# Kernel optimization log

Hardware: AMD Instinct MI355X
Metric: run time of the kernel (lower is better)

## Reference

```python
import jax, jax.numpy as jnp
import numpy as np

V, N, C, H, W = 4, 65536, 128, 512, 512
M_POOL, K, DH = 1024, 5, 128


def setup_inputs() -> dict:
    key = jax.random.key(0)
    ks = jax.random.split(key, 6)
    points = jax.random.normal(ks[0], (N, 3), dtype=jnp.float32) * 0.3  # human-scale pcd near origin
    zbuffer = 2.0 + jax.random.uniform(ks[1], (V, 1, H, W), dtype=jnp.float32)  # depth ~ camera distance
    feat_map = jax.random.normal(ks[2], (V, C, H, W), dtype=jnp.float32) * 0.1
    image = jax.random.uniform(ks[3], (V, 3, H, W), dtype=jnp.float32)
    # cameras: identity rotation, small x-baseline, looking at origin from z=2.5
    R = jnp.tile(jnp.eye(3, dtype=jnp.float32)[None], (V, 1, 1))
    t = jnp.stack([jnp.array([0.1 * v - 0.15, 0.0, 2.5], dtype=jnp.float32) for v in range(V)])
    extr = jnp.concatenate([R, t[:, :, None]], axis=-1)  # [V,3,4]
    intr = jnp.tile(jnp.array([[700.0, 0.0, W / 2], [0.0, 700.0, H / 2], [0.0, 0.0, 1.0]], dtype=jnp.float32)[None], (V, 1, 1))
    W1 = jax.random.normal(ks[4], (C + 1, DH), dtype=jnp.float32) * 0.05
    b1 = jnp.zeros((DH,), dtype=jnp.float32)
    w2 = jax.random.normal(ks[5], (DH, 1), dtype=jnp.float32) * 0.05
    return dict(points=points, extr=extr, intr=intr, zbuffer=zbuffer,
                feat_map=feat_map, image=image, W1=W1, b1=b1, w2=w2)


def _bilinear(img, u, v):
    """Zero-padded bilinear sample. img [C,H,W]; u,v [N] pixel coords -> [N,C]."""
    Cc, Hh, Ww = img.shape
    u0f = jnp.floor(u); v0f = jnp.floor(v)
    du = u - u0f; dv = v - v0f
    u0 = u0f.astype(jnp.int32); v0 = v0f.astype(jnp.int32)
    out = jnp.zeros((Cc, u.shape[0]), dtype=img.dtype)
    for vi, ui, w in ((v0, u0, (1 - du) * (1 - dv)), (v0, u0 + 1, du * (1 - dv)),
                      (v0 + 1, u0, (1 - du) * dv), (v0 + 1, u0 + 1, du * dv)):
        valid = ((vi >= 0) & (vi < Hh) & (ui >= 0) & (ui < Ww)).astype(img.dtype)
        vals = img[:, jnp.clip(vi, 0, Hh - 1), jnp.clip(ui, 0, Ww - 1)]  # [C,N]
        out = out + vals * (w * valid)[None]
    return out.T  # [N,C]


def _project(points, extr, intr):
    cam = jnp.einsum('vij,nj->vni', extr[:, :, :3], points) + extr[:, None, :, 3]  # [V,N,3]
    depth = cam[..., 2]  # [V,N]
    pix = jnp.einsum('vij,vnj->vni', intr, cam)
    u = pix[..., 0] / (pix[..., 2] + 1e-9)
    v = pix[..., 1] / (pix[..., 2] + 1e-9)
    return u, v, depth


def reference(points, extr, intr, zbuffer, feat_map, image, W1, b1, w2):
    u, v, depth = _project(points, extr, intr)
    sample = jax.vmap(_bilinear)  # over V views
    zbuf = sample(zbuffer, u, v)[..., 0]  # [V,N] sampled z-buffer (0 outside frame)
    out_mask = jnp.any(zbuf == 0.0, axis=0)  # [N] point missing in some view
    # --- KNN inverse-distance zbuf replacement (torch.no_grad block) ---
    pts_sg = jax.lax.stop_gradient(points)
    zbuf_sg = jax.lax.stop_gradient(zbuf)
    cand = pts_sg[:M_POOL]                       # candidate in-point pool
    cand_bad = out_mask[:M_POOL]
    d2 = jnp.sum((pts_sg[:, None, :] - cand[None, :, :]) ** 2, axis=-1)  # [N,M]
    d2 = jnp.where(cand_bad[None, :], jnp.inf, d2)
    negd, idx = jax.lax.top_k(-d2, K)            # K nearest candidates
    dists = jnp.sqrt(jnp.maximum(-negd, 0.0))
    disp = 1.0 / (dists + 1e-8)
    wknn = disp / (jnp.sum(disp, -1, keepdims=True) + 1e-12)  # [N,K]
    replace = jnp.sum(zbuf_sg[:, idx] * wknn[None], -1)       # [V,N]
    zbuf = jnp.where(out_mask[None], replace, zbuf)
    # --- visibility ---
    vis = 1.0 - jnp.abs(zbuf - depth) / (zbuf + 1e-9)  # [V,N]
    # --- multi-view projector sampling + attention fusion (MVF) ---
    feat_s = sample(feat_map, u, v)  # [V,N,C]
    rgb_s = sample(image, u, v)      # [V,N,3]
    x = jnp.concatenate([feat_s, vis[..., None]], -1)          # [V,N,C+1]
    h = jax.nn.relu(jnp.einsum('vnc,cd->vnd', x, W1) + b1)     # [V,N,DH]
    attn = jax.nn.softmax(jnp.einsum('vnd,do->vno', h, w2), axis=0)  # softmax over views
    feat = jnp.sum(attn * feat_s, axis=0)  # [N,C]
    rgb = jnp.sum(attn * rgb_s, axis=0)    # [N,3]
    return jnp.concatenate([feat, rgb], axis=-1)  # [N,C+3]
```

## Files before the change

### kernel.cpp

```cpp
#include <hip/hip_runtime.h>
#include <math.h>

#define NV 4
#define NPT 65536
#define NC 128
#define IMH 512
#define IMW 512
#define MPOOL 1024
#define NDH 128
#define KNN 5
#define NB 8
#define OUTC 131
#define NFLAGS (4 * 512 * 4)

typedef unsigned int uint32;
typedef unsigned short ushort16;
typedef __attribute__((ext_vector_type(8))) short short8v;
typedef __attribute__((ext_vector_type(4))) float float4v;

__device__ inline ushort16 f2bf(float f) {
    uint32 u = __float_as_uint(f);
    u += 0x7fffu + ((u >> 16) & 1u);
    return (ushort16)(u >> 16);
}
__device__ inline float bflo(uint32 a) { return __uint_as_float(a << 16); }
__device__ inline float bfhi(uint32 a) { return __uint_as_float(a & 0xffff0000u); }
__device__ inline float bf1(ushort16 a) { return __uint_as_float(((uint32)a) << 16); }

__global__ void k_wprep(const float* __restrict__ W1, uint4* __restrict__ Bf,
                        int* __restrict__ counter, int* __restrict__ flags) {
    int idx = blockIdx.x * blockDim.x + threadIdx.x;
    if (idx == 0) *counter = 0;
    if (idx < NFLAGS) flags[idx] = 0;
    if (idx >= 5 * 8 * 64) return;
    int l = idx & 63, t = (idx >> 6) & 7, kb = idx >> 9;
    int d = t * 16 + (l & 15);
    uint32 w[4];
#pragma unroll
    for (int p = 0; p < 4; ++p) {
        uint32 lohi = 0;
#pragma unroll
        for (int h = 0; h < 2; ++h) {
            int j = p * 2 + h;
            int k = kb * 32 + (l >> 4) * 8 + j;
            float wv = (k < NC + 1) ? W1[k * NDH + d] : 0.f;
            lohi |= ((uint32)f2bf(wv)) << (16 * h);
        }
        w[p] = lohi;
    }
    Bf[idx] = make_uint4(w[0], w[1], w[2], w[3]);
}

__global__ __launch_bounds__(256)
void k_prep(const float* __restrict__ pts, const float* __restrict__ extr,
            const float* __restrict__ intr, const float* __restrict__ zbuffer,
            float* __restrict__ uarr, float* __restrict__ varr,
            float* __restrict__ darr, float* __restrict__ zarr,
            int* __restrict__ mask, int* __restrict__ list,
            int* __restrict__ counter, int* __restrict__ flags) {
    int n = blockIdx.x * blockDim.x + threadIdx.x;
    if (n >= NPT) return;
    float p0 = pts[3 * n], p1 = pts[3 * n + 1], p2 = pts[3 * n + 2];
    int msk = 0;
#pragma unroll
    for (int v = 0; v < NV; ++v) {
        const float* e = extr + v * 12;
        float c0 = e[0] * p0 + e[1] * p1 + e[2] * p2 + e[3];
        float c1 = e[4] * p0 + e[5] * p1 + e[6] * p2 + e[7];
        float c2 = e[8] * p0 + e[9] * p1 + e[10] * p2 + e[11];
        const float* kk = intr + v * 9;
        float x0 = kk[0] * c0 + kk[1] * c1 + kk[2] * c2;
        float x1 = kk[3] * c0 + kk[4] * c1 + kk[5] * c2;
        float x2 = kk[6] * c0 + kk[7] * c1 + kk[8] * c2;
        float uu = x0 / (x2 + 1e-9f);
        float vv = x1 / (x2 + 1e-9f);
        int vn = v * NPT + n;
        uarr[vn] = uu; varr[vn] = vv; darr[vn] = c2;

        const float* img = zbuffer + (size_t)v * IMH * IMW;
        float u0f = floorf(uu), v0f = floorf(vv);
        float du = uu - u0f, dv = vv - v0f;
        int iu0 = (int)u0f, iv0 = (int)v0f;
        float w00 = (1.f - du) * (1.f - dv);
        float w01 = du * (1.f - dv);
        float w10 = (1.f - du) * dv;
        float w11 = du * dv;
        int iu0c = min(max(iu0, 0), IMW - 1), iu1c = min(max(iu0 + 1, 0), IMW - 1);
        int iv0c = min(max(iv0, 0), IMH - 1), iv1c = min(max(iv0 + 1, 0), IMH - 1);
        float m00 = (iu0 >= 0 && iu0 < IMW && iv0 >= 0 && iv0 < IMH) ? w00 : 0.f;
        float m01 = (iu0 + 1 >= 0 && iu0 + 1 < IMW && iv0 >= 0 && iv0 < IMH) ? w01 : 0.f;
        float m10 = (iu0 >= 0 && iu0 < IMW && iv0 + 1 >= 0 && iv0 + 1 < IMH) ? w10 : 0.f;
        float m11 = (iu0 + 1 >= 0 && iu0 + 1 < IMW && iv0 + 1 >= 0 && iv0 + 1 < IMH) ? w11 : 0.f;
        float z = img[iv0c * IMW + iu0c] * m00 + img[iv0c * IMW + iu1c] * m01 +
                  img[iv1c * IMW + iu0c] * m10 + img[iv1c * IMW + iu1c] * m11;
        zarr[vn] = z;
        msk |= (z == 0.f);

        int base = v * 2048;
        int xt0 = iu0c >> 7, xt1 = iu1c >> 7;
        flags[base + iv0c * 4 + xt0] = 1;
        flags[base + iv0c * 4 + xt1] = 1;
        flags[base + iv1c * 4 + xt0] = 1;
        flags[base + iv1c * 4 + xt1] = 1;
    }
    mask[n] = msk;
    if (msk) {
        int pos = atomicAdd(counter, 1);
        list[pos] = n;
    }
}

__global__ __launch_bounds__(256)
void k_knn_c(const float* __restrict__ pts, const int* __restrict__ mask,
             const int* __restrict__ list, const int* __restrict__ counter,
             float* __restrict__ zarr) {
    __shared__ float cx[MPOOL], cy[MPOOL], cz[MPOOL];
    int count = *counter;
    if ((int)blockIdx.x * 256 >= count) return;
    for (int m = threadIdx.x; m < MPOOL; m += 256) {
        int bad = mask[m];
        cx[m] = bad ? INFINITY : pts[3 * m];
        cy[m] = pts[3 * m + 1];
        cz[m] = pts[3 * m + 2];
    }
    __syncthreads();
    int i = blockIdx.x * 256 + threadIdx.x;
    if (i >= count) return;
    int n = list[i];
    float px = pts[3 * n], py = pts[3 * n + 1], pz = pts[3 * n + 2];
    float bd[KNN];
    int bi[KNN];
#pragma unroll
    for (int k = 0; k < KNN; ++k) { bd[k] = INFINITY; bi[k] = 0; }
    for (int m = 0; m < MPOOL; ++m) {
        float dx = px - cx[m];
        float dy = py - cy[m];
        float dz = pz - cz[m];
        float d = dx * dx + dy * dy + dz * dz;
        int id = m;
#pragma unroll
        for (int k = 0; k < KNN; ++k) {
            if (d < bd[k]) {
                float td = bd[k]; int ti = bi[k];
                bd[k] = d; bi[k] = id;
                d = td; id = ti;
            }
        }
    }
    float disp[KNN];
    float s = 0.f;
#pragma unroll
    for (int k = 0; k < KNN; ++k) {
        float dist = sqrtf(fmaxf(bd[k], 0.f));
        disp[k] = 1.f / (dist + 1e-8f);
        s += disp[k];
    }
    float inv = 1.f / (s + 1e-12f);
#pragma unroll
    for (int v = 0; v < NV; ++v) {
        float r = 0.f;
#pragma unroll
        for (int k = 0; k < KNN; ++k) r += zarr[v * NPT + bi[k]] * (disp[k] * inv);
        zarr[v * NPT + n] = r;
    }
}

__global__ __launch_bounds__(256)
void k_tfeat(const float* __restrict__ feat, ushort16* __restrict__ tfeat,
             const int* __restrict__ flags) {
    __shared__ ushort16 tile[128][130];
    int bid = blockIdx.x;
    int xt = bid & 3;
    int y = (bid >> 2) & 511;
    int v = bid >> 11;
    if (!flags[v * 2048 + y * 4 + xt]) return;
    int x0 = xt * 128;
    int lane = threadIdx.x & 63, wave = threadIdx.x >> 6;
    const size_t HW = (size_t)IMH * IMW;
    const float* src = feat + (size_t)v * NC * HW + (size_t)y * IMW + x0;
#pragma unroll
    for (int i = 0; i < 32; ++i) {
        int c = i * 4 + wave;
        float2 val = *(const float2*)(src + (size_t)c * HW + lane * 2);
        tile[lane * 2][c] = f2bf(val.x);
        tile[lane * 2 + 1][c] = f2bf(val.y);
    }
    __syncthreads();
    uint32* dst = (uint32*)tfeat + ((size_t)v * HW + (size_t)y * IMW + x0) * 64;
#pragma unroll
    for (int i = 0; i < 32; ++i) {
        int pix = i * 4 + wave;
        uint32 val = *(const uint32*)&tile[pix][2 * lane];
        dst[(size_t)pix * 64 + lane] = val;
    }
}

__global__ __launch_bounds__(256)
void k_trgb(const float* __restrict__ image, ushort16* __restrict__ trgb) {
    int bid = blockIdx.x;
    int xt = bid & 1, y = (bid >> 1) & 511, v = bid >> 10;
    int x = xt * 256 + threadIdx.x;
    const size_t HW = (size_t)IMH * IMW;
    size_t p = (size_t)y * IMW + x;
    const float* src = image + (size_t)v * 3 * HW;
    ushort4 o;
    o.x = f2bf(src[p]);
    o.y = f2bf(src[HW + p]);
    o.z = f2bf(src[2 * HW + p]);
    o.w = 0;
    *(ushort4*)(trgb + ((size_t)v * HW + p) * 4) = o;
}

__global__ __launch_bounds__(128)
void k_fused_m(const float* __restrict__ uarr, const float* __restrict__ varr,
               const float* __restrict__ darr, const float* __restrict__ zarr,
               const ushort16* __restrict__ tfeat, const ushort16* __restrict__ trgb,
               const uint4* __restrict__ Bf, const float* __restrict__ b1,
               const float* __restrict__ w2, float* __restrict__ out) {
    const int tid = threadIdx.x;
    const int n0 = blockIdx.x * NB;
    const size_t HW = (size_t)IMH * IMW;
    __shared__ ushort16 fs[32][168];
    __shared__ float rgbs[32][3];
    __shared__ int po[32][4];
    __shared__ float pm[32][4];
    __shared__ float sc[32];
    __shared__ float red[32][2];

    {
        int q = tid >> 2, corner = tid & 3;
        int nb = q >> 2, v = q & 3;
        int vn = v * NPT + n0 + nb;
        float uu = uarr[vn], vv = varr[vn];
        float u0f = floorf(uu), v0f = floorf(vv);
        float du = uu - u0f, dv = vv - v0f;
        int iu0 = (int)u0f, iv0 = (int)v0f;
        float w00 = (1.f - du) * (1.f - dv);
        float w01 = du * (1.f - dv);
        float w10 = (1.f - du) * dv;
        float w11 = du * dv;
        int iu0c = min(max(iu0, 0), IMW - 1), iu1c = min(max(iu0 + 1, 0), IMW - 1);
        int iv0c = min(max(iv0, 0), IMH - 1), iv1c = min(max(iv0 + 1, 0), IMH - 1);
        float m00 = (iu0 >= 0 && iu0 < IMW && iv0 >= 0 && iv0 < IMH) ? w00 : 0.f;
        float m01 = (iu0 + 1 < IMW && iu0 + 1 >= 0 && iv0 >= 0 && iv0 < IMH) ? w01 : 0.f;
        float m10 = (iu0 >= 0 && iu0 < IMW && iv0 + 1 < IMH && iv0 + 1 >= 0) ? w10 : 0.f;
        float m11 = (iu0 + 1 < IMW && iu0 + 1 >= 0 && iv0 + 1 < IMH && iv0 + 1 >= 0) ? w11 : 0.f;
        int oo, iuc, ivc;
        float mm;
        if (corner == 0)      { ivc = iv0c; iuc = iu0c; mm = m00; }
        else if (corner == 1) { ivc = iv0c; iuc = iu1c; mm = m01; }
        else if (corner == 2) { ivc = iv1c; iuc = iu0c; mm = m10; }
        else                  { ivc = iv1c; iuc = iu1c; mm = m11; }
        oo = ivc * IMW + iuc;
        po[q][corner] = oo;
        pm[q][corner] = mm;
        const ushort16* c = trgb + ((size_t)v * HW + oo) * 4;
        float cr = bf1(c[0]) * mm, cg = bf1(c[1]) * mm, cb = bf1(c[2]) * mm;
        cr += __shfl_xor(cr, 1); cr += __shfl_xor(cr, 2);
        cg += __shfl_xor(cg, 1); cg += __shfl_xor(cg, 2);
        cb += __shfl_xor(cb, 1); cb += __shfl_xor(cb, 2);
        if (corner == 0) {
            rgbs[q][0] = cr; rgbs[q][1] = cg; rgbs[q][2] = cb;
            float z = zarr[vn], dd = darr[vn];
            float vis = 1.f - fabsf(z - dd) / (z + 1e-9f);
            fs[q][128] = f2bf(vis);
        }
        for (int k = 129 + corner; k < 168; k += 4) fs[q][k] = 0;
    }
    __syncthreads();

    const uint32* T = (const uint32*)tfeat;
    int sub = tid >> 6, c2 = tid & 63;
#pragma unroll
    for (int i = 0; i < 16; ++i) {
        int q = i * 2 + sub;
        int v = q & 3;
        const uint32* Bv = T + (size_t)v * HW * 64;
        int o0 = po[q][0], o1 = po[q][1], o2 = po[q][2], o3 = po[q][3];
        float m0 = pm[q][0], m1 = pm[q][1], m2 = pm[q][2], m3 = pm[q][3];
        uint32 a0 = Bv[(size_t)o0 * 64 + c2];
        uint32 a1 = Bv[(size_t)o1 * 64 + c2];
        uint32 a2 = Bv[(size_t)o2 * 64 + c2];
        uint32 a3 = Bv[(size_t)o3 * 64 + c2];
        float lo = bflo(a0) * m0 + bflo(a1) * m1 + bflo(a2) * m2 + bflo(a3) * m3;
        float hi = bfhi(a0) * m0 + bfhi(a1) * m1 + bfhi(a2) * m2 + bfhi(a3) * m3;
        uint32 packed = (uint32)f2bf(lo) | ((uint32)f2bf(hi) << 16);
        *(uint32*)&fs[q][2 * c2] = packed;
    }
    __syncthreads();

    const int l = tid & 63, w = tid >> 6;
    const int col = l & 15, kg = l >> 4;
    float4v acc[2][4];
#pragma unroll
    for (int g = 0; g < 2; ++g)
#pragma unroll
        for (int t = 0; t < 4; ++t) acc[g][t] = (float4v){0.f, 0.f, 0.f, 0.f};
#pragma unroll
    for (int kb = 0; kb < 5; ++kb) {
        short8v a0 = *(const short8v*)&fs[col][kb * 32 + kg * 8];
        short8v a1 = *(const short8v*)&fs[16 + col][kb * 32 + kg * 8];
#pragma unroll
        for (int tt = 0; tt < 4; ++tt) {
            int t = w * 4 + tt;
            short8v bv = *(const short8v*)&Bf[(kb * 8 + t) * 64 + l];
            acc[0][tt] = __builtin_amdgcn_mfma_f32_16x16x32_bf16(a0, bv, acc[0][tt], 0, 0, 0);
            acc[1][tt] = __builtin_amdgcn_mfma_f32_16x16x32_bf16(a1, bv, acc[1][tt], 0, 0, 0);
        }
    }
    float bias[4], w2v[4];
#pragma unroll
    for (int tt = 0; tt < 4; ++tt) {
        int d = (w * 4 + tt) * 16 + col;
        bias[tt] = b1[d];
        w2v[tt] = w2[d];
    }
    float p[2][4] = {{0.f, 0.f, 0.f, 0.f}, {0.f, 0.f, 0.f, 0.f}};
#pragma unroll
    for (int g = 0; g < 2; ++g)
#pragma unroll
        for (int tt = 0; tt < 4; ++tt)
#pragma unroll
            for (int r = 0; r < 4; ++r)
                p[g][r] += fmaxf(acc[g][tt][r] + bias[tt], 0.f) * w2v[tt];
#pragma unroll
    for (int m = 1; m < 16; m <<= 1)
#pragma unroll
        for (int g = 0; g < 2; ++g)
#pragma unroll
            for (int r = 0; r < 4; ++r) p[g][r] += __shfl_xor(p[g][r], m);
    if (col == 0) {
#pragma unroll
        for (int g = 0; g < 2; ++g)
#pragma unroll
            for (int r = 0; r < 4; ++r) red[g * 16 + kg * 4 + r][w] = p[g][r];
    }
    __syncthreads();
    if (tid < 32) sc[tid] = red[tid][0] + red[tid][1];
    __syncthreads();
    if (tid < NB) {
        float s0 = sc[tid * 4 + 0], s1 = sc[tid * 4 + 1];
        float s2 = sc[tid * 4 + 2], s3 = sc[tid * 4 + 3];
        float mx = fmaxf(fmaxf(s0, s1), fmaxf(s2, s3));
        float e0 = expf(s0 - mx), e1 = expf(s1 - mx);
        float e2 = expf(s2 - mx), e3 = expf(s3 - mx);
        float inv = 1.f / (e0 + e1 + e2 + e3);
        sc[tid * 4 + 0] = e0 * inv; sc[tid * 4 + 1] = e1 * inv;
        sc[tid * 4 + 2] = e2 * inv; sc[tid * 4 + 3] = e3 * inv;
    }
    __syncthreads();

#pragma unroll
    for (int nb = 0; nb < NB; ++nb) {
        int n = n0 + nb;
        float f = 0.f;
#pragma unroll
        for (int v = 0; v < NV; ++v) f += sc[nb * 4 + v] * bf1(fs[nb * 4 + v][tid]);
        out[(size_t)n * OUTC + tid] = f;
        if (tid < 3) {
            float r = 0.f;
#pragma unroll
            for (int v = 0; v < NV; ++v) r += sc[nb * 4 + v] * rgbs[nb * 4 + v][tid];
            out[(size_t)n * OUTC + NC + tid] = r;
        }
    }
}

__global__ __launch_bounds__(128)
void k_fused_d(const float* __restrict__ uarr, const float* __restrict__ varr,
               const float* __restrict__ darr, const float* __restrict__ zarr,
               const float* __restrict__ feat, const float* __restrict__ image,
               const float* __restrict__ W1, const float* __restrict__ b1,
               const float* __restrict__ w2, float* __restrict__ out) {
    const int tid = threadIdx.x;
    const int n0 = blockIdx.x * 4;
    __shared__ float fs[4][NV][NC];
    __shared__ float rgbs[4][NV][3];
    __shared__ float sc[4][NV];
    __shared__ float red[4][NV][2];
    float vis[4][NV];

#pragma unroll
    for (int nb = 0; nb < 4; ++nb) {
        int n = n0 + nb;
#pragma unroll
        for (int v = 0; v < NV; ++v) {
            int vn = v * NPT + n;
            float uu = uarr[vn], vv = varr[vn];
            float u0f = floorf(uu), v0f = floorf(vv);
            float du = uu - u0f, dv = vv - v0f;
            int iu0 = (int)u0f, iv0 = (int)v0f;
            float w00 = (1.f - du) * (1.f - dv);
            float w01 = du * (1.f - dv);
            float w10 = (1.f - du) * dv;
            float w11 = du * dv;
            int iu0c = min(max(iu0, 0), IMW - 1), iu1c = min(max(iu0 + 1, 0), IMW - 1);
            int iv0c = min(max(iv0, 0), IMH - 1), iv1c = min(max(iv0 + 1, 0), IMH - 1);
            float m00 = (iu0 >= 0 && iu0 < IMW && iv0 >= 0 && iv0 < IMH) ? w00 : 0.f;
            float m01 = (iu0 + 1 < IMW && iu0 + 1 >= 0 && iv0 >= 0 && iv0 < IMH) ? w01 : 0.f;
            float m10 = (iu0 >= 0 && iu0 < IMW && iv0 + 1 < IMH && iv0 + 1 >= 0) ? w10 : 0.f;
            float m11 = (iu0 + 1 < IMW && iu0 + 1 >= 0 && iv0 + 1 < IMH && iv0 + 1 >= 0) ? w11 : 0.f;
            int o00 = iv0c * IMW + iu0c, o01 = iv0c * IMW + iu1c;
            int o10 = iv1c * IMW + iu0c, o11 = iv1c * IMW + iu1c;
            const float* base = feat + ((size_t)(v * NC + tid)) * IMH * IMW;
            fs[nb][v][tid] = base[o00] * m00 + base[o01] * m01 +
                             base[o10] * m10 + base[o11] * m11;
            if (tid < 3) {
                const float* ib = image + ((size_t)(v * 3 + tid)) * IMH * IMW;
                rgbs[nb][v][tid] = ib[o00] * m00 + ib[o01] * m01 +
                                   ib[o10] * m10 + ib[o11] * m11;
            }
            float z = zarr[vn], dd = darr[vn];
            vis[nb][v] = 1.f - fabsf(z - dd) / (z + 1e-9f);
        }
    }
    __syncthreads();

    float h[4][NV];
    float bv = b1[tid];
#pragma unroll
    for (int nb = 0; nb < 4; ++nb)
#pragma unroll
        for (int v = 0; v < NV; ++v) h[nb][v] = bv;
    for (int c = 0; c < NC; ++c) {
        float w = W1[c * NDH + tid];
#pragma unroll
        for (int nb = 0; nb < 4; ++nb)
#pragma unroll
            for (int v = 0; v < NV; ++v) h[nb][v] = fmaf(fs[nb][v][c], w, h[nb][v]);
    }
    {
        float w = W1[NC * NDH + tid];
#pragma unroll
        for (int nb = 0; nb < 4; ++nb)
#pragma unroll
            for (int v = 0; v < NV; ++v) h[nb][v] = fmaf(vis[nb][v], w, h[nb][v]);
    }
    float w2t = w2[tid];
    int lane = tid & 63, wave = tid >> 6;
#pragma unroll
    for (int nb = 0; nb < 4; ++nb) {
#pragma unroll
        for (int v = 0; v < NV; ++v) {
            float p = fmaxf(h[nb][v], 0.f) * w2t;
#pragma unroll
            for (int off = 32; off > 0; off >>= 1) p += __shfl_down(p, off);
            if (lane == 0) red[nb][v][wave] = p;
        }
    }
    __syncthreads();
    if (tid < 16) {
        int nb = tid >> 2, v = tid & 3;
        sc[nb][v] = red[nb][v][0] + red[nb][v][1];
    }
    __syncthreads();
    if (tid < 4) {
        float s0 = sc[tid][0], s1 = sc[tid][1], s2 = sc[tid][2], s3 = sc[tid][3];
        float mx = fmaxf(fmaxf(s0, s1), fmaxf(s2, s3));
        float e0 = expf(s0 - mx), e1 = expf(s1 - mx);
        float e2 = expf(s2 - mx), e3 = expf(s3 - mx);
        float inv = 1.f / (e0 + e1 + e2 + e3);
        sc[tid][0] = e0 * inv; sc[tid][1] = e1 * inv;
        sc[tid][2] = e2 * inv; sc[tid][3] = e3 * inv;
    }
    __syncthreads();
#pragma unroll
    for (int nb = 0; nb < 4; ++nb) {
        int n = n0 + nb;
        float f = 0.f;
#pragma unroll
        for (int v = 0; v < NV; ++v) f += sc[nb][v] * fs[nb][v][tid];
        out[(size_t)n * OUTC + tid] = f;
        if (tid < 3) {
            float r = 0.f;
#pragma unroll
            for (int v = 0; v < NV; ++v) r += sc[nb][v] * rgbs[nb][v][tid];
            out[(size_t)n * OUTC + NC + tid] = r;
        }
    }
}

extern "C" void kernel_launch(void* const* d_in, const int* in_sizes, int n_in,
                              void* d_out, int out_size, void* d_ws, size_t ws_size,
                              hipStream_t stream) {
    const float* pts = (const float*)d_in[0];
    const float* extr = (const float*)d_in[1];
    const float* intr = (const float*)d_in[2];
    const float* zbuffer = (const float*)d_in[3];
    const float* feat = (const float*)d_in[4];
    const float* image = (const float*)d_in[5];
    const float* W1 = (const float*)d_in[6];
    const float* b1 = (const float*)d_in[7];
    const float* w2 = (const float*)d_in[8];
    float* out = (float*)d_out;

    const size_t VN = (size_t)NV * NPT;
    float* uarr = (float*)d_ws;
    float* varr = uarr + VN;
    float* darr = varr + VN;
    float* zarr = darr + VN;
    int* mask = (int*)(zarr + VN);
    int* list = mask + NPT;
    int* counter = list + NPT;
    int* flags = counter + 16;
    uint4* Bf = (uint4*)(flags + NFLAGS);
    char* after = (char*)(Bf + 5 * 8 * 64);
    ushort16* trgb = (ushort16*)after;
    ushort16* tfeat = (ushort16*)(after + (size_t)NV * IMH * IMW * 4 * 2);
    size_t need = (size_t)((char*)tfeat - (char*)d_ws) + (size_t)NV * IMH * IMW * NC * 2;

    k_wprep<<<32, 256, 0, stream>>>(W1, Bf, counter, flags);
    k_prep<<<NPT / 256, 256, 0, stream>>>(pts, extr, intr, zbuffer,
                                          uarr, varr, darr, zarr,
                                          mask, list, counter, flags);
    k_knn_c<<<NPT / 256, 256, 0, stream>>>(pts, mask, list, counter, zarr);

    if (ws_size >= need) {
        k_tfeat<<<NV * 512 * 4, 256, 0, stream>>>(feat, tfeat, flags);
        k_trgb<<<NV * 512 * 2, 256, 0, stream>>>(image, trgb);
        k_fused_m<<<NPT / NB, 128, 0, stream>>>(uarr, varr, darr, zarr, tfeat, trgb,
                                                Bf, b1, w2, out);
    } else {
        k_fused_d<<<NPT / 4, 128, 0, stream>>>(uarr, varr, darr, zarr, feat, image,
                                               W1, b1, w2, out);
    }
}
```

Baseline: 468.9 us.

## Sort points by image cell for gather locality and fold RGB transpose into feature kernel

Points are binned by their view-0 pixel cell (32x32 tiles) using a counting sort: counts in k_prep, a scan kernel and a scatter kernel that build a permutation. The fused kernel then walks points in this order, with workgroups interleaved across eight slices, so neighbouring points gather nearby feature texels and hit in cache. The separate RGB conversion kernel is merged into the feature transpose kernel, which only runs for tiles that points touch. This adds three small kernels plus atomics and an indirection load. The merged RGB conversion now skips tiles no point samples, which matches how those tiles are actually read.

```diff
diff --git a/kernel.cpp b/kernel.cpp
--- a/kernel.cpp
+++ b/kernel.cpp
@@ -12,6 +12,7 @@
 #define NB 8
 #define OUTC 131
 #define NFLAGS (4 * 512 * 4)
+#define NCELL 256
 
 typedef unsigned int uint32;
 typedef unsigned short ushort16;
@@ -28,10 +29,12 @@
 __device__ inline float bf1(ushort16 a) { return __uint_as_float(((uint32)a) << 16); }
 
 __global__ void k_wprep(const float* __restrict__ W1, uint4* __restrict__ Bf,
-                        int* __restrict__ counter, int* __restrict__ flags) {
+                        int* __restrict__ counter, int* __restrict__ flags,
+                        int* __restrict__ cellcnt) {
     int idx = blockIdx.x * blockDim.x + threadIdx.x;
     if (idx == 0) *counter = 0;
     if (idx < NFLAGS) flags[idx] = 0;
+    if (idx < NCELL) cellcnt[idx] = 0;
     if (idx >= 5 * 8 * 64) return;
     int l = idx & 63, t = (idx >> 6) & 7, kb = idx >> 9;
     int d = t * 16 + (l & 15);
@@ -57,7 +60,8 @@
             float* __restrict__ uarr, float* __restrict__ varr,
             float* __restrict__ darr, float* __restrict__ zarr,
             int* __restrict__ mask, int* __restrict__ list,
-            int* __restrict__ counter, int* __restrict__ flags) {
+            int* __restrict__ counter, int* __restrict__ flags,
+            int* __restrict__ celli, int* __restrict__ cellcnt) {
     int n = blockIdx.x * blockDim.x + threadIdx.x;
     if (n >= NPT) return;
     float p0 = pts[3 * n], p1 = pts[3 * n + 1], p2 = pts[3 * n + 2];
@@ -102,12 +106,44 @@
         flags[base + iv0c * 4 + xt1] = 1;
         flags[base + iv1c * 4 + xt0] = 1;
         flags[base + iv1c * 4 + xt1] = 1;
+
+        if (v == 0) {
+            int cell = (iv0c >> 5) * 16 + (iu0c >> 5);
+            celli[n] = cell;
+            atomicAdd(&cellcnt[cell], 1);
+        }
     }
     mask[n] = msk;
     if (msk) {
         int pos = atomicAdd(counter, 1);
         list[pos] = n;
     }
+}
+
+__global__ __launch_bounds__(256)
+void k_scan(const int* __restrict__ cellcnt, int* __restrict__ cellofs) {
+    __shared__ int s[NCELL];
+    int t = threadIdx.x;
+    int c = cellcnt[t];
+    s[t] = c;
+    __syncthreads();
+#pragma unroll
+    for (int off = 1; off < NCELL; off <<= 1) {
+        int vv = (t >= off) ? s[t - off] : 0;
+        __syncthreads();
+        s[t] += vv;
+        __syncthreads();
+    }
+    cellofs[t] = s[t] - c;
+}
+
+__global__ __launch_bounds__(256)
+void k_scat(const int* __restrict__ celli, int* __restrict__ cellofs,
+            int* __restrict__ perm) {
+    int n = blockIdx.x * blockDim.x + threadIdx.x;
+    if (n >= NPT) return;
+    int pos = atomicAdd(&cellofs[celli[n]], 1);
+    perm[pos] = n;
 }
 
 __global__ __launch_bounds__(256)
@@ -167,6 +203,7 @@
 
 __global__ __launch_bounds__(256)
 void k_tfeat(const float* __restrict__ feat, ushort16* __restrict__ tfeat,
+             const float* __restrict__ image, ushort16* __restrict__ trgb,
              const int* __restrict__ flags) {
     __shared__ ushort16 tile[128][130];
     int bid = blockIdx.x;
@@ -185,6 +222,17 @@
         tile[lane * 2][c] = f2bf(val.x);
         tile[lane * 2 + 1][c] = f2bf(val.y);
     }
+    if (threadIdx.x < 128) {
+        int px = threadIdx.x;
+        size_t p = (size_t)y * IMW + x0 + px;
+        const float* isrc = image + (size_t)v * 3 * HW;
+        ushort4 o;
+        o.x = f2bf(isrc[p]);
+        o.y = f2bf(isrc[HW + p]);
+        o.z = f2bf(isrc[2 * HW + p]);
+        o.w = 0;
+        *(ushort4*)(trgb + ((size_t)v * HW + p) * 4) = o;
+    }
     __syncthreads();
     uint32* dst = (uint32*)tfeat + ((size_t)v * HW + (size_t)y * IMW + x0) * 64;
 #pragma unroll
@@ -193,22 +241,6 @@
         uint32 val = *(const uint32*)&tile[pix][2 * lane];
         dst[(size_t)pix * 64 + lane] = val;
     }
-}
-
-__global__ __launch_bounds__(256)
-void k_trgb(const float* __restrict__ image, ushort16* __restrict__ trgb) {
-    int bid = blockIdx.x;
-    int xt = bid & 1, y = (bid >> 1) & 511, v = bid >> 10;
-    int x = xt * 256 + threadIdx.x;
-    const size_t HW = (size_t)IMH * IMW;
-    size_t p = (size_t)y * IMW + x;
-    const float* src = image + (size_t)v * 3 * HW;
-    ushort4 o;
-    o.x = f2bf(src[p]);
-    o.y = f2bf(src[HW + p]);
-    o.z = f2bf(src[2 * HW + p]);
-    o.w = 0;
-    *(ushort4*)(trgb + ((size_t)v * HW + p) * 4) = o;
 }
 
 __global__ __launch_bounds__(128)
@@ -216,10 +248,13 @@
                const float* __restrict__ darr, const float* __restrict__ zarr,
                const ushort16* __restrict__ tfeat, const ushort16* __restrict__ trgb,
                const uint4* __restrict__ Bf, const float* __restrict__ b1,
-               const float* __restrict__ w2, float* __restrict__ out) {
+               const float* __restrict__ w2, const int* __restrict__ perm,
+               float* __restrict__ out) {
     const int tid = threadIdx.x;
-    const int n0 = blockIdx.x * NB;
+    const int wg = (blockIdx.x & 7) * (NPT / NB / 8) + (blockIdx.x >> 3);
+    const int n0 = wg * NB;
     const size_t HW = (size_t)IMH * IMW;
+    __shared__ int pn[NB];
     __shared__ ushort16 fs[32][168];
     __shared__ float rgbs[32][3];
     __shared__ int po[32][4];
@@ -227,10 +262,13 @@
     __shared__ float sc[32];
     __shared__ float red[32][2];
 
+    if (tid < NB) pn[tid] = perm[n0 + tid];
+    __syncthreads();
+
     {
         int q = tid >> 2, corner = tid & 3;
         int nb = q >> 2, v = q & 3;
-        int vn = v * NPT + n0 + nb;
+        int vn = v * NPT + pn[nb];
         float uu = uarr[vn], vv = varr[vn];
         float u0f = floorf(uu), v0f = floorf(vv);
         float du = uu - u0f, dv = vv - v0f;
@@ -352,7 +390,7 @@
 
 #pragma unroll
     for (int nb = 0; nb < NB; ++nb) {
-        int n = n0 + nb;
+        int n = pn[nb];
         float f = 0.f;
 #pragma unroll
         for (int v = 0; v < NV; ++v) f += sc[nb * 4 + v] * bf1(fs[nb * 4 + v][tid]);
@@ -503,23 +541,29 @@
     int* list = mask + NPT;
     int* counter = list + NPT;
     int* flags = counter + 16;
-    uint4* Bf = (uint4*)(flags + NFLAGS);
+    int* celli = flags + NFLAGS;
+    int* perm = celli + NPT;
+    int* cellcnt = perm + NPT;
+    int* cellofs = cellcnt + NCELL;
+    uint4* Bf = (uint4*)(cellofs + NCELL);
     char* after = (char*)(Bf + 5 * 8 * 64);
     ushort16* trgb = (ushort16*)after;
     ushort16* tfeat = (ushort16*)(after + (size_t)NV * IMH * IMW * 4 * 2);
     size_t need = (size_t)((char*)tfeat - (char*)d_ws) + (size_t)NV * IMH * IMW * NC * 2;
 
-    k_wprep<<<32, 256, 0, stream>>>(W1, Bf, counter, flags);
+    k_wprep<<<32, 256, 0, stream>>>(W1, Bf, counter, flags, cellcnt);
     k_prep<<<NPT / 256, 256, 0, stream>>>(pts, extr, intr, zbuffer,
                                           uarr, varr, darr, zarr,
-                                          mask, list, counter, flags);
+                                          mask, list, counter, flags,
+                                          celli, cellcnt);
+    k_scan<<<1, 256, 0, stream>>>(cellcnt, cellofs);
+    k_scat<<<NPT / 256, 256, 0, stream>>>(celli, cellofs, perm);
     k_knn_c<<<NPT / 256, 256, 0, stream>>>(pts, mask, list, counter, zarr);
 
     if (ws_size >= need) {
-        k_tfeat<<<NV * 512 * 4, 256, 0, stream>>>(feat, tfeat, flags);
-        k_trgb<<<NV * 512 * 2, 256, 0, stream>>>(image, trgb);
+        k_tfeat<<<NV * 512 * 4, 256, 0, stream>>>(feat, tfeat, image, trgb, flags);
         k_fused_m<<<NPT / NB, 128, 0, stream>>>(uarr, varr, darr, zarr, tfeat, trgb,
-                                                Bf, b1, w2, out);
+                                                Bf, b1, w2, perm, out);
     } else {
         k_fused_d<<<NPT / 4, 128, 0, stream>>>(uarr, varr, darr, zarr, feat, image,
                                                W1, b1, w2, out);
```

New measurement: 595.9 us. +27.1%, slower.

## Drop tile-skip flags and RGB pre-transpose; widen feature loads and gathers

Applied to the files above, without the earlier changes.

Removes the per-tile occupancy flags, so k_tfeat now transposes the entire feature map to bf16 rather than only the rows touched by projected points. It also drops the RGB transpose kernel and reads fp32 image channels directly in the fused kernel. The feature transpose switches to float4 loads, and the bilinear feature gather uses 16-byte per-lane loads with fewer threads per point. The flag removal gives up work skipping and adds full-map transpose traffic (the projected points likely cover only a small region). In exchange it removes the flag atomics/stores and one launch.

```diff
diff --git a/kernel.cpp b/kernel.cpp
--- a/kernel.cpp
+++ b/kernel.cpp
@@ -11,7 +11,6 @@
 #define KNN 5
 #define NB 8
 #define OUTC 131
-#define NFLAGS (4 * 512 * 4)
 
 typedef unsigned int uint32;
 typedef unsigned short ushort16;
@@ -28,10 +27,9 @@
 __device__ inline float bf1(ushort16 a) { return __uint_as_float(((uint32)a) << 16); }
 
 __global__ void k_wprep(const float* __restrict__ W1, uint4* __restrict__ Bf,
-                        int* __restrict__ counter, int* __restrict__ flags) {
+                        int* __restrict__ counter) {
     int idx = blockIdx.x * blockDim.x + threadIdx.x;
     if (idx == 0) *counter = 0;
-    if (idx < NFLAGS) flags[idx] = 0;
     if (idx >= 5 * 8 * 64) return;
     int l = idx & 63, t = (idx >> 6) & 7, kb = idx >> 9;
     int d = t * 16 + (l & 15);
@@ -57,7 +55,7 @@
             float* __restrict__ uarr, float* __restrict__ varr,
             float* __restrict__ darr, float* __restrict__ zarr,
             int* __restrict__ mask, int* __restrict__ list,
-            int* __restrict__ counter, int* __restrict__ flags) {
+            int* __restrict__ counter) {
     int n = blockIdx.x * blockDim.x + threadIdx.x;
     if (n >= NPT) return;
     float p0 = pts[3 * n], p1 = pts[3 * n + 1], p2 = pts[3 * n + 2];
@@ -95,13 +93,6 @@
                   img[iv1c * IMW + iu0c] * m10 + img[iv1c * IMW + iu1c] * m11;
         zarr[vn] = z;
         msk |= (z == 0.f);
-
-        int base = v * 2048;
-        int xt0 = iu0c >> 7, xt1 = iu1c >> 7;
-        flags[base + iv0c * 4 + xt0] = 1;
-        flags[base + iv0c * 4 + xt1] = 1;
-        flags[base + iv1c * 4 + xt0] = 1;
-        flags[base + iv1c * 4 + xt1] = 1;
     }
     mask[n] = msk;
     if (msk) {
@@ -166,24 +157,26 @@
 }
 
 __global__ __launch_bounds__(256)
-void k_tfeat(const float* __restrict__ feat, ushort16* __restrict__ tfeat,
-             const int* __restrict__ flags) {
+void k_tfeat(const float* __restrict__ feat, ushort16* __restrict__ tfeat) {
     __shared__ ushort16 tile[128][130];
     int bid = blockIdx.x;
     int xt = bid & 3;
     int y = (bid >> 2) & 511;
     int v = bid >> 11;
-    if (!flags[v * 2048 + y * 4 + xt]) return;
     int x0 = xt * 128;
     int lane = threadIdx.x & 63, wave = threadIdx.x >> 6;
+    int half = lane >> 5, l5 = lane & 31;
     const size_t HW = (size_t)IMH * IMW;
     const float* src = feat + (size_t)v * NC * HW + (size_t)y * IMW + x0;
 #pragma unroll
-    for (int i = 0; i < 32; ++i) {
-        int c = i * 4 + wave;
-        float2 val = *(const float2*)(src + (size_t)c * HW + lane * 2);
-        tile[lane * 2][c] = f2bf(val.x);
-        tile[lane * 2 + 1][c] = f2bf(val.y);
+    for (int i = 0; i < 16; ++i) {
+        int c = i * 8 + wave * 2 + half;
+        float4 val = *(const float4*)(src + (size_t)c * HW + l5 * 4);
+        int px = l5 * 4;
+        tile[px + 0][c] = f2bf(val.x);
+        tile[px + 1][c] = f2bf(val.y);
+        tile[px + 2][c] = f2bf(val.z);
+        tile[px + 3][c] = f2bf(val.w);
     }
     __syncthreads();
     uint32* dst = (uint32*)tfeat + ((size_t)v * HW + (size_t)y * IMW + x0) * 64;
@@ -195,26 +188,10 @@
     }
 }
 
-__global__ __launch_bounds__(256)
-void k_trgb(const float* __restrict__ image, ushort16* __restrict__ trgb) {
-    int bid = blockIdx.x;
-    int xt = bid & 1, y = (bid >> 1) & 511, v = bid >> 10;
-    int x = xt * 256 + threadIdx.x;
-    const size_t HW = (size_t)IMH * IMW;
-    size_t p = (size_t)y * IMW + x;
-    const float* src = image + (size_t)v * 3 * HW;
-    ushort4 o;
-    o.x = f2bf(src[p]);
-    o.y = f2bf(src[HW + p]);
-    o.z = f2bf(src[2 * HW + p]);
-    o.w = 0;
-    *(ushort4*)(trgb + ((size_t)v * HW + p) * 4) = o;
-}
-
 __global__ __launch_bounds__(128)
 void k_fused_m(const float* __restrict__ uarr, const float* __restrict__ varr,
                const float* __restrict__ darr, const float* __restrict__ zarr,
-               const ushort16* __restrict__ tfeat, const ushort16* __restrict__ trgb,
+               const ushort16* __restrict__ tfeat, const float* __restrict__ image,
                const uint4* __restrict__ Bf, const float* __restrict__ b1,
                const float* __restrict__ w2, float* __restrict__ out) {
     const int tid = threadIdx.x;
@@ -245,17 +222,17 @@
         float m01 = (iu0 + 1 < IMW && iu0 + 1 >= 0 && iv0 >= 0 && iv0 < IMH) ? w01 : 0.f;
         float m10 = (iu0 >= 0 && iu0 < IMW && iv0 + 1 < IMH && iv0 + 1 >= 0) ? w10 : 0.f;
         float m11 = (iu0 + 1 < IMW && iu0 + 1 >= 0 && iv0 + 1 < IMH && iv0 + 1 >= 0) ? w11 : 0.f;
-        int oo, iuc, ivc;
+        int iuc, ivc;
         float mm;
         if (corner == 0)      { ivc = iv0c; iuc = iu0c; mm = m00; }
         else if (corner == 1) { ivc = iv0c; iuc = iu1c; mm = m01; }
         else if (corner == 2) { ivc = iv1c; iuc = iu0c; mm = m10; }
         else                  { ivc = iv1c; iuc = iu1c; mm = m11; }
-        oo = ivc * IMW + iuc;
+        int oo = ivc * IMW + iuc;
         po[q][corner] = oo;
         pm[q][corner] = mm;
-        const ushort16* c = trgb + ((size_t)v * HW + oo) * 4;
-        float cr = bf1(c[0]) * mm, cg = bf1(c[1]) * mm, cb = bf1(c[2]) * mm;
+        const float* ib = image + (size_t)v * 3 * HW + oo;
+        float cr = ib[0] * mm, cg = ib[HW] * mm, cb = ib[2 * HW] * mm;
         cr += __shfl_xor(cr, 1); cr += __shfl_xor(cr, 2);
         cg += __shfl_xor(cg, 1); cg += __shfl_xor(cg, 2);
         cb += __shfl_xor(cb, 1); cb += __shfl_xor(cb, 2);
@@ -270,22 +247,32 @@
     __syncthreads();
 
     const uint32* T = (const uint32*)tfeat;
-    int sub = tid >> 6, c2 = tid & 63;
-#pragma unroll
-    for (int i = 0; i < 16; ++i) {
-        int q = i * 2 + sub;
-        int v = q & 3;
-        const uint32* Bv = T + (size_t)v * HW * 64;
-        int o0 = po[q][0], o1 = po[q][1], o2 = po[q][2], o3 = po[q][3];
-        float m0 = pm[q][0], m1 = pm[q][1], m2 = pm[q][2], m3 = pm[q][3];
-        uint32 a0 = Bv[(size_t)o0 * 64 + c2];
-        uint32 a1 = Bv[(size_t)o1 * 64 + c2];
-        uint32 a2 = Bv[(size_t)o2 * 64 + c2];
-        uint32 a3 = Bv[(size_t)o3 * 64 + c2];
-        float lo = bflo(a0) * m0 + bflo(a1) * m1 + bflo(a2) * m2 + bflo(a3) * m3;
-        float hi = bfhi(a0) * m0 + bfhi(a1) * m1 + bfhi(a2) * m2 + bfhi(a3) * m3;
-        uint32 packed = (uint32)f2bf(lo) | ((uint32)f2bf(hi) << 16);
-        *(uint32*)&fs[q][2 * c2] = packed;
+    {
+        int wv = tid >> 6, l = tid & 63;
+        int ql = l >> 4, g = l & 15;
+#pragma unroll
+        for (int i = 0; i < 4; ++i) {
+            int q = i * 8 + wv * 4 + ql;
+            int v = q & 3;
+            const uint32* Bv = T + (size_t)v * HW * 64;
+            float a0 = 0.f, a1 = 0.f, a2 = 0.f, a3 = 0.f;
+            float a4 = 0.f, a5 = 0.f, a6 = 0.f, a7 = 0.f;
+#pragma unroll
+            for (int k = 0; k < 4; ++k) {
+                uint4 A = *(const uint4*)(Bv + (size_t)po[q][k] * 64 + g * 4);
+                float m = pm[q][k];
+                a0 += bflo(A.x) * m; a1 += bfhi(A.x) * m;
+                a2 += bflo(A.y) * m; a3 += bfhi(A.y) * m;
+                a4 += bflo(A.z) * m; a5 += bfhi(A.z) * m;
+                a6 += bflo(A.w) * m; a7 += bfhi(A.w) * m;
+            }
+            uint4 r;
+            r.x = (uint32)f2bf(a0) | ((uint32)f2bf(a1) << 16);
+            r.y = (uint32)f2bf(a2) | ((uint32)f2bf(a3) << 16);
+            r.z = (uint32)f2bf(a4) | ((uint32)f2bf(a5) << 16);
+            r.w = (uint32)f2bf(a6) | ((uint32)f2bf(a7) << 16);
+            *(uint4*)&fs[q][g * 8] = r;
+        }
     }
     __syncthreads();
 
@@ -502,23 +489,20 @@
     int* mask = (int*)(zarr + VN);
     int* list = mask + NPT;
     int* counter = list + NPT;
-    int* flags = counter + 16;
-    uint4* Bf = (uint4*)(flags + NFLAGS);
+    uint4* Bf = (uint4*)(counter + 16);
     char* after = (char*)(Bf + 5 * 8 * 64);
-    ushort16* trgb = (ushort16*)after;
-    ushort16* tfeat = (ushort16*)(after + (size_t)NV * IMH * IMW * 4 * 2);
+    ushort16* tfeat = (ushort16*)after;
     size_t need = (size_t)((char*)tfeat - (char*)d_ws) + (size_t)NV * IMH * IMW * NC * 2;
 
-    k_wprep<<<32, 256, 0, stream>>>(W1, Bf, counter, flags);
+    k_wprep<<<10, 256, 0, stream>>>(W1, Bf, counter);
     k_prep<<<NPT / 256, 256, 0, stream>>>(pts, extr, intr, zbuffer,
                                           uarr, varr, darr, zarr,
-                                          mask, list, counter, flags);
+                                          mask, list, counter);
     k_knn_c<<<NPT / 256, 256, 0, stream>>>(pts, mask, list, counter, zarr);
 
     if (ws_size >= need) {
-        k_tfeat<<<NV * 512 * 4, 256, 0, stream>>>(feat, tfeat, flags);
-        k_trgb<<<NV * 512 * 2, 256, 0, stream>>>(image, trgb);
-        k_fused_m<<<NPT / NB, 128, 0, stream>>>(uarr, varr, darr, zarr, tfeat, trgb,
+        k_tfeat<<<NV * 512 * 4, 256, 0, stream>>>(feat, tfeat);
+        k_fused_m<<<NPT / NB, 128, 0, stream>>>(uarr, varr, darr, zarr, tfeat, image,
                                                 Bf, b1, w2, out);
     } else {
         k_fused_d<<<NPT / 4, 128, 0, stream>>>(uarr, varr, darr, zarr, feat, image,
```

New measurement: 472.2 us. Within noise of the previous version (+0.7%).
